# Kernel optimization log

Measured on AMD Instinct MI355X. Metric: run time of the kernel, lower is better.

## Reference

```python
import jax, jax.numpy as jnp
import numpy as np

EPS = 1e-5


def layer_norm(x, g, b):
    m = jnp.mean(x, axis=-1, keepdims=True)
    v = jnp.mean((x - m) ** 2, axis=-1, keepdims=True)
    return (x - m) / jnp.sqrt(v + EPS) * g + b


def rel_shift(x, klen):
    # x: [q, p, b, n] -> Transformer-XL relative shift -> [q, klen, b, n]
    q, p, b, n = x.shape
    x = jnp.reshape(x, (p, q, b, n))
    x = x[1:]
    x = jnp.reshape(x, (q, p - 1, b, n))
    return x[:, :klen]


def setup_inputs() -> dict:
    S, B, D, NH, DH, DF = 1024, 4, 1024, 16, 64, 4096
    key = jax.random.key(0)
    ks = jax.random.split(key, 16)
    w = 0.02  # scale random params for numerical sanity
    return {
        "src": jax.random.normal(ks[0], (S, B, D), jnp.float32),
        "pos_emb": jax.random.normal(ks[1], (S + 1, B, D), jnp.float32),
        "src_mask": jnp.zeros((S, S), dtype=bool),
        "qw": jax.random.normal(ks[2], (D, NH, DH), jnp.float32) * w,
        "kw": jax.random.normal(ks[3], (D, NH, DH), jnp.float32) * w,
        "vw": jax.random.normal(ks[4], (D, NH, DH), jnp.float32) * w,
        "rw": jax.random.normal(ks[5], (D, NH, DH), jnp.float32) * w,
        "ow": jax.random.normal(ks[6], (D, NH, DH), jnp.float32) * w,
        "r_w_bias": jax.random.normal(ks[7], (NH, DH), jnp.float32) * w,
        "r_r_bias": jax.random.normal(ks[8], (NH, DH), jnp.float32) * w,
        "w1": jax.random.normal(ks[9], (DF, D), jnp.float32) * w,
        "b1": jnp.zeros((DF,), jnp.float32),
        "w2": jax.random.normal(ks[10], (D, DF), jnp.float32) * w,
        "b2": jnp.zeros((D,), jnp.float32),
        "g1": jnp.ones((D,), jnp.float32),
        "beta1": jnp.zeros((D,), jnp.float32),
        "g2": jnp.ones((D,), jnp.float32),
        "beta2": jnp.zeros((D,), jnp.float32),
    }


def reference(src, pos_emb, src_mask, qw, kw, vw, rw, ow, r_w_bias, r_r_bias,
              w1, b1, w2, b2, g1, beta1, g2, beta2):
    S = src.shape[0]
    d_head = qw.shape[-1]
    scale = 1.0 / d_head ** 0.5

    # mem=None -> cat == src; dropout layers are identity (eval)
    q_head = jnp.einsum('ibh,hnd->ibnd', src, qw)
    k_head = jnp.einsum('ibh,hnd->ibnd', src, kw)
    v_head = jnp.einsum('ibh,hnd->ibnd', src, vw)
    k_pos = jnp.einsum('ibh,hnd->ibnd', pos_emb, rw)

    ac = jnp.einsum('ibnd,jbnd->ijbn', q_head + r_w_bias, k_head)       # [S,S,B,N]
    bd = jnp.einsum('ibnd,jbnd->ijbn', q_head + r_r_bias, k_pos)        # [S,S+1,B,N]
    bd = rel_shift(bd, klen=S)

    mask = src_mask.astype(ac.dtype)[:, :, None, None]
    attn_score = (ac + bd) * scale - 1e30 * mask
    attn_prob = jax.nn.softmax(attn_score, axis=1)

    attn_vec = jnp.einsum('ijbn,jbnd->ibnd', attn_prob, v_head)
    attn_out = jnp.einsum('ibnd,hnd->ibh', attn_vec, ow)

    x = layer_norm(src + attn_out, g1, beta1)
    ff = jax.nn.gelu(x @ w1.T + b1, approximate=False) @ w2.T + b2
    return layer_norm(x + ff, g2, beta2)
```

## Files before the change

### kernel.cpp

```cpp
#include <hip/hip_runtime.h>
#include <math.h>

typedef __bf16 bf16x8 __attribute__((ext_vector_type(8)));
typedef __bf16 bf16x4 __attribute__((ext_vector_type(4)));
typedef float f32x4 __attribute__((ext_vector_type(4)));

__device__ __forceinline__ void gload_lds16(const __bf16* g, __bf16* l) {
  __builtin_amdgcn_global_load_lds((const __attribute__((address_space(1))) void*)g,
                                   (__attribute__((address_space(3))) void*)l, 16, 0, 0);
}

__device__ __forceinline__ float gelu_exact(float v) {
  return 0.5f * v * (1.f + erff(v * 0.70710678118654752f));
}

__global__ __launch_bounds__(256) void prep_all(
    const float* __restrict__ src, __bf16* __restrict__ srcB2,
    const float* __restrict__ pos, __bf16* __restrict__ posB,
    const float* __restrict__ ow, __bf16* __restrict__ owB,
    const float* __restrict__ w1, __bf16* __restrict__ w1B,
    const float* __restrict__ w2, __bf16* __restrict__ w2B,
    const float* __restrict__ qw, const float* __restrict__ kw,
    const float* __restrict__ vw, const float* __restrict__ rw,
    __bf16* __restrict__ qkvT, __bf16* __restrict__ rwT) {
  __shared__ float t[32][33];
  int bid = blockIdx.x;
  const int tid = threadIdx.x;
  if (bid < 4096) {
    const int i = bid & 1023, b = bid >> 10;
    const float4 v = *(const float4*)(src + ((size_t)(i * 4 + b)) * 1024 + tid * 4);
    bf16x4 o = {(__bf16)v.x, (__bf16)v.y, (__bf16)v.z, (__bf16)v.w};
    *(bf16x4*)(srcB2 + (size_t)bid * 1024 + tid * 4) = o;
    return;
  }
  bid -= 4096;
  if (bid < 3329) {
    const float* in; __bf16* out;
    if (bid < 1025) { in = pos; out = posB; }
    else if (bid < 1281) { bid -= 1025; in = ow; out = owB; }
    else if (bid < 2305) { bid -= 1281; in = w1; out = w1B; }
    else { bid -= 2305; in = w2; out = w2B; }
    const int base = bid * 4096 + tid * 4;
#pragma unroll
    for (int k2 = 0; k2 < 4; ++k2) {
      const int off = base + k2 * 1024;
      float4 v = *(const float4*)(in + off);
      bf16x4 o = {(__bf16)v.x, (__bf16)v.y, (__bf16)v.z, (__bf16)v.w};
      *(bf16x4*)(out + off) = o;
    }
    return;
  }
  bid -= 3329;
  const int z = bid >> 10, rem = bid & 1023;
  const float* in; __bf16* out;
  switch (z) {
    case 0: in = qw; out = qkvT; break;
    case 1: in = kw; out = qkvT + 1024 * 1024; break;
    case 2: in = vw; out = qkvT + 2048 * 1024; break;
    default: in = rw; out = rwT; break;
  }
  const int c0 = (rem & 31) * 32, r0 = (rem >> 5) * 32;
  const int tx = tid & 31, ty = tid >> 5;
  for (int yy = ty; yy < 32; yy += 8)
    t[yy][tx] = in[(size_t)(r0 + yy) * 1024 + c0 + tx];
  __syncthreads();
  for (int yy = ty; yy < 32; yy += 8)
    out[(size_t)(c0 + yy) * 1024 + r0 + tx] = (__bf16)t[tx][yy];
}

template<int BM, int BN, int MODE>
__device__ __forceinline__ void gemm_body(
    const __bf16* __restrict__ A, const __bf16* __restrict__ BT,
    float* __restrict__ Cf, __bf16* __restrict__ Cb,
    const float* __restrict__ bias, int M, int N, int K,
    int kStart, int kChunk, int mBase, int nBase, char* smemRaw) {
  constexpr int BK = 32;
  constexpr int ALOAD = (BM * BK) / 2048;
  constexpr int BLOAD = (BN * BK) / 2048;
  __bf16* lA = (__bf16*)smemRaw;
  __bf16* lB = (__bf16*)(smemRaw + 4 * BM * BK);
  const int tid = threadIdx.x;
  const int w = tid >> 6, l = tid & 63;
  const int lr = l & 15, lk = l >> 4;
  const int srow = tid >> 2;
  const int scol = (tid & 3) * 8;
  const int wbase = w * 512;

  const __bf16* aSrc[ALOAD];
  const __bf16* bSrc[BLOAD];
#pragma unroll
  for (int i = 0; i < ALOAD; ++i) {
    int grow = mBase + srow + i * 64;
    grow = grow < M ? grow : M - 1;
    aSrc[i] = A + (size_t)grow * K + kStart + scol;
  }
#pragma unroll
  for (int i = 0; i < BLOAD; ++i) {
    const int grow = nBase + srow + i * 64;
    bSrc[i] = BT + (size_t)grow * K + kStart + scol;
  }
  auto stage = [&](int buf) {
#pragma unroll
    for (int i = 0; i < ALOAD; ++i) {
      gload_lds16(aSrc[i], &lA[buf * BM * BK + i * 2048 + wbase]);
      aSrc[i] += BK;
    }
#pragma unroll
    for (int i = 0; i < BLOAD; ++i) {
      gload_lds16(bSrc[i], &lB[buf * BN * BK + i * 2048 + wbase]);
      bSrc[i] += BK;
    }
  };

  constexpr int WM = BM / 2, WN = BN / 2;
  constexpr int MF = WM / 16, NF = WN / 16;
  const int wr = w >> 1, wc = w & 1;
  f32x4 acc[MF][NF] = {};

  const int nIter = kChunk / BK;
  stage(0);
  int cur = 0;
#pragma unroll 1
  for (int t = 0; t < nIter; ++t) {
    __syncthreads();
    if (t + 1 < nIter) stage(cur ^ 1);
    bf16x8 af[MF], bfr[NF];
#pragma unroll
    for (int mi = 0; mi < MF; ++mi)
      af[mi] = *(const bf16x8*)&lA[cur * BM * BK + (wr * WM + mi * 16 + lr) * BK + lk * 8];
#pragma unroll
    for (int nj = 0; nj < NF; ++nj)
      bfr[nj] = *(const bf16x8*)&lB[cur * BN * BK + (wc * WN + nj * 16 + lr) * BK + lk * 8];
#pragma unroll
    for (int mi = 0; mi < MF; ++mi)
#pragma unroll
      for (int nj = 0; nj < NF; ++nj)
        acc[mi][nj] = __builtin_amdgcn_mfma_f32_16x16x32_bf16(af[mi], bfr[nj], acc[mi][nj], 0, 0, 0);
    cur ^= 1;
  }
#pragma unroll
  for (int mi = 0; mi < MF; ++mi) {
#pragma unroll
    for (int nj = 0; nj < NF; ++nj) {
      const int col = nBase + wc * WN + nj * 16 + lr;
      const int row0 = mBase + wr * WM + mi * 16 + lk * 4;
#pragma unroll
      for (int j = 0; j < 4; ++j) {
        const int row = row0 + j;
        if (row < M) {
          float v = acc[mi][nj][j];
          if constexpr (MODE == 1) {
            v = gelu_exact(v + bias[col]);
            Cb[(size_t)row * N + col] = (__bf16)v;
          } else if constexpr (MODE == 2) {
            Cb[(size_t)row * N + col] = (__bf16)v;
          } else {
            Cf[(size_t)row * N + col] = v;
          }
        }
      }
    }
  }
}

template<int BM, int BN, int MODE>
__global__ __launch_bounds__(256)
void gemm_bt(const __bf16* __restrict__ A, const __bf16* __restrict__ BT,
             float* __restrict__ Cf, __bf16* __restrict__ Cb,
             __bf16* __restrict__ Cb2, const float* __restrict__ bias,
             int M, int N, int K, int kChunk) {
  __shared__ __align__(16) char smem[4 * (BM + BN) * 32];
  __bf16* cb = (blockIdx.z == 1) ? Cb2 : Cb;
  const int gx = gridDim.x;
  const int G = gx * gridDim.y;
  const int flat = blockIdx.y * gx + blockIdx.x;
  const int band = G >> 3;
  const int x8 = flat & 7, loc = flat >> 3;
  const int rpb = band / gx;
  const int ny = x8 * rpb + loc % rpb;
  const int nx = loc / rpb;
  gemm_body<BM, BN, MODE>(A, BT, Cf, cb, bias, M, N, K, blockIdx.z * kChunk,
                          kChunk, ny * BM, nx * BN, smem);
}

__global__ __launch_bounds__(256)
void proj3_kernel(const __bf16* __restrict__ srcB2, const __bf16* __restrict__ qkvT,
                  const __bf16* __restrict__ vwT, const __bf16* __restrict__ posB,
                  const __bf16* __restrict__ rwT, __bf16* __restrict__ qkB,
                  __bf16* __restrict__ vTB, __bf16* __restrict__ kposB) {
  __shared__ __align__(16) char smem[4 * (128 + 64) * 32];
  const int raw = blockIdx.x;
  int bid = (raw & 7) * 258 + (raw >> 3);
  if (bid < 1024) {
    gemm_body<128, 64, 2>(srcB2, qkvT, nullptr, qkB, nullptr, 4096, 2048, 1024,
                          0, 1024, (bid >> 5) * 128, (bid & 31) * 64, smem);
  } else if (bid < 1536) {
    const int t = bid - 1024;
    gemm_body<128, 64, 2>(vwT, srcB2, nullptr, vTB, nullptr, 1024, 4096, 1024,
                          0, 1024, (t >> 6) * 128, (t & 63) * 64, smem);
  } else {
    const int t = bid - 1536;
    gemm_body<128, 64, 2>(posB, rwT, nullptr, kposB, nullptr, 4100, 1024, 1024,
                          0, 1024, (t >> 4) * 128, (t & 15) * 64, smem);
  }
}

__global__ __launch_bounds__(256)
void attn8(const __bf16* __restrict__ qk, const __bf16* __restrict__ vT,
           const __bf16* __restrict__ kpos, const float* __restrict__ rwbias,
           const float* __restrict__ rrbias, __bf16* __restrict__ av) {
  constexpr float ALPHA = 0.125f * 1.44269504088896f;
  constexpr int PB = 132;
  __shared__ __align__(16) char smem[74240];
  __bf16* sP  = (__bf16*)(smem + 49152);
  __bf16* sbd = (__bf16*)(smem + 57344);

  const int flat = blockIdx.x;
  const int xcd = flat & 7, rr_ = flat >> 3;
  const int bn = xcd * 8 + (rr_ >> 4);
  const int it = rr_ & 15;
  const int b = bn >> 4, n = bn & 15;
  const int i0 = it * 64;
  const int tid = threadIdx.x;
  const int l = tid & 63;
  const int lcol = l & 15, lk = l >> 4;
  const int strip = (tid >> 6) * 16;
  const int wbase = tid & 192;
  const int nh64 = n * 64;
  const int q = strip + lcol;

  const int rB = tid >> 3;
  const int cs8 = ((tid & 7) ^ (rB & 7)) * 8;

  bf16x8 onesf;
#pragma unroll
  for (int u = 0; u < 8; ++u) onesf[u] = (__bf16)1.0f;

  bf16x8 qac[2], qlo[2], qhi[2];
  {
    const __bf16* qrow = qk + ((size_t)(b * 1024 + i0 + q)) * 2048 + nh64;
    int gH = i0 + q + 1; gH = gH < 1024 ? gH : 1023;
    const __bf16* qrowH = qk + ((size_t)(b * 1024 + gH)) * 2048 + nh64;
#pragma unroll
    for (int kk = 0; kk < 2; ++kk) {
      bf16x8 qv = *(const bf16x8*)(qrow + kk * 32 + lk * 8);
      bf16x8 qh = *(const bf16x8*)(qrowH + kk * 32 + lk * 8);
      const int dbase = nh64 + kk * 32 + lk * 8;
#pragma unroll
      for (int u = 0; u < 8; ++u) {
        const float rb = rrbias[dbase + u];
        qac[kk][u] = (__bf16)(((float)qv[u] + rwbias[dbase + u]) * ALPHA);
        qlo[kk][u] = (__bf16)(((float)qv[u] + rb) * ALPHA);
        qhi[kk][u] = (__bf16)(((float)qh[u] + rb) * ALPHA);
      }
    }
  }

#pragma unroll
  for (int kq = 0; kq < 2; ++kq) {
    const int r = kq * 32 + rB;
    const int dst = (kq * 256 + wbase) * 8;
    gload_lds16(kpos + ((size_t)((960 - i0 + r) * 4 + b)) * 1024 + nh64 + cs8,
                (__bf16*)(smem + 40960) + dst);
    gload_lds16(qk + ((size_t)(b * 1024 + r)) * 2048 + 1024 + nh64 + cs8,
                (__bf16*)(smem) + dst);
    const int rrel = r - i0;
    const int idx = (rrel <= 0) ? (1024 + rrel) : (rrel - 1);
    gload_lds16(kpos + ((size_t)(idx * 4 + b)) * 1024 + nh64 + cs8,
                (__bf16*)(smem + 16384) + dst);
    gload_lds16(vT + ((size_t)(nh64 + r)) * 4096 + b * 1024 + cs8,
                (__bf16*)(smem + 32768) + dst);
  }
  __syncthreads();
  {
    __bf16* kpl = (__bf16*)(smem + 40960);
    const int colb0 = (-i0 - 64) & 127;
#pragma unroll
    for (int fb = 0; fb < 4; ++fb) {
      const int row = fb * 16 + lcol;
      f32x4 g = {};
#pragma unroll
      for (int kk = 0; kk < 2; ++kk) {
        bf16x8 a = *(const bf16x8*)&kpl[row * 64 + (((kk * 4 + lk) ^ (lcol & 7)) * 8)];
        g = __builtin_amdgcn_mfma_f32_16x16x32_bf16(a, qlo[kk], g, 0, 0, 0);
      }
      bf16x4 gw = {(__bf16)g[0], (__bf16)g[1], (__bf16)g[2], (__bf16)g[3]};
      *(bf16x4*)&sbd[q * PB + ((colb0 + fb * 16 + lk * 4) & 127)] = gw;
    }
  }
  __syncthreads();

  f32x4 oacc[4] = {};
  f32x4 zq = {};
  size_t kS = (size_t)(b * 1024 + 64 + rB) * 2048 + 1024 + nh64 + cs8;
  size_t vS = (size_t)(nh64 + rB) * 4096 + b * 1024 + 64 + cs8;

#pragma unroll 1
  for (int jt = 0; jt < 16; ++jt) {
    const int cur = jt & 1, nxt = cur ^ 1;
    const int d0 = jt * 64 - i0;
    __bf16* sK   = (__bf16*)(smem + cur * 8192);
    __bf16* sKn  = (__bf16*)(smem + nxt * 8192);
    __bf16* sKP  = (__bf16*)(smem + 16384 + cur * 8192);
    __bf16* sKPn = (__bf16*)(smem + 16384 + nxt * 8192);
    __bf16* sVT  = (__bf16*)(smem + 32768 + cur * 8192);
    __bf16* sVTn = (__bf16*)(smem + 32768 + nxt * 8192);
#pragma unroll
    for (int kq = 0; kq < 2; ++kq) {
      const int dst = (kq * 256 + wbase) * 8;
      gload_lds16(qk + kS + kq * 65536, sKn + dst);
      gload_lds16(vT + vS + kq * 131072, sVTn + dst);
      const int rreln = d0 + 64 + kq * 32 + rB;
      const int idx = (rreln <= 0) ? (1024 + rreln) : (rreln - 1);
      gload_lds16(kpos + ((size_t)(idx * 4 + b)) * 1024 + nh64 + cs8, sKPn + dst);
    }
    kS += 131072; vS += 64;
    {
      const bf16x8 qg0 = (d0 >= 0) ? qhi[0] : qlo[0];
      const bf16x8 qg1 = (d0 >= 0) ? qhi[1] : qlo[1];
#pragma unroll
      for (int fb = 0; fb < 4; ++fb) {
        const int row = fb * 16 + lcol;
        f32x4 g = {};
        g = __builtin_amdgcn_mfma_f32_16x16x32_bf16(
            *(const bf16x8*)&sKP[row * 64 + ((lk ^ (lcol & 7)) * 8)], qg0, g, 0, 0, 0);
        g = __builtin_amdgcn_mfma_f32_16x16x32_bf16(
            *(const bf16x8*)&sKP[row * 64 + (((4 + lk) ^ (lcol & 7)) * 8)], qg1, g, 0, 0, 0);
        bf16x4 gw = {(__bf16)g[0], (__bf16)g[1], (__bf16)g[2], (__bf16)g[3]};
        *(bf16x4*)&sbd[q * PB + ((d0 + fb * 16 + lk * 4) & 127)] = gw;
      }
      if (d0 == 0) {
        const int cl = tid >> 2, part = tid & 3;
        const __bf16* qs = qk + ((size_t)(b * 1024 + i0 + cl)) * 2048 + nh64 + part * 16;
        bf16x8 a0 = *(const bf16x8*)qs;
        bf16x8 a1 = *(const bf16x8*)(qs + 8);
        bf16x8 k0 = *(const bf16x8*)&sKP[(2 * part) * 8];
        bf16x8 k1 = *(const bf16x8*)&sKP[(2 * part + 1) * 8];
        float s64 = 0.f;
#pragma unroll
        for (int u = 0; u < 8; ++u)
          s64 += ((float)a0[u] + rrbias[nh64 + part * 16 + u]) * (float)k0[u]
               + ((float)a1[u] + rrbias[nh64 + part * 16 + 8 + u]) * (float)k1[u];
        s64 += __shfl_xor(s64, 1, 64);
        s64 += __shfl_xor(s64, 2, 64);
        if (part == 0) sbd[cl * PB] = (__bf16)(s64 * ALPHA);
      }
    }
    f32x4 sc[4];
#pragma unroll
    for (int fk = 0; fk < 4; ++fk) {
      const int row = fk * 16 + lcol;
      f32x4 a = {};
#pragma unroll
      for (int kk = 0; kk < 2; ++kk) {
        bf16x8 kf = *(const bf16x8*)&sK[row * 64 + (((kk * 4 + lk) ^ (lcol & 7)) * 8)];
        a = __builtin_amdgcn_mfma_f32_16x16x32_bf16(kf, qac[kk], a, 0, 0, 0);
      }
      sc[fk] = a;
    }
    {
      const int rowb = q * PB;
      const int sb = d0 - q;
#pragma unroll
      for (int fk = 0; fk < 4; ++fk) {
        const int cb = sb + fk * 16 + lk * 4;
        float e0 = exp2f(sc[fk][0] + (float)sbd[rowb + ((cb) & 127)]);
        float e1 = exp2f(sc[fk][1] + (float)sbd[rowb + ((cb + 1) & 127)]);
        float e2 = exp2f(sc[fk][2] + (float)sbd[rowb + ((cb + 2) & 127)]);
        float e3 = exp2f(sc[fk][3] + (float)sbd[rowb + ((cb + 3) & 127)]);
        bf16x4 pw = {(__bf16)e0, (__bf16)e1, (__bf16)e2, (__bf16)e3};
        *(bf16x4*)&sP[q * 64 + (((fk * 2 + (lk >> 1)) ^ (q & 7)) * 8) + (lk & 1) * 4] = pw;
      }
    }
#pragma unroll
    for (int kk = 0; kk < 2; ++kk) {
      bf16x8 pa = *(const bf16x8*)&sP[q * 64 + (((kk * 4 + lk) ^ (q & 7)) * 8)];
      zq = __builtin_amdgcn_mfma_f32_16x16x32_bf16(pa, onesf, zq, 0, 0, 0);
#pragma unroll
      for (int fd = 0; fd < 4; ++fd) {
        const int vrow = fd * 16 + lcol;
        bf16x8 bv = *(const bf16x8*)&sVT[vrow * 64 + (((kk * 4 + lk) ^ (lcol & 7)) * 8)];
        oacc[fd] = __builtin_amdgcn_mfma_f32_16x16x32_bf16(pa, bv, oacc[fd], 0, 0, 0);
      }
    }
    __syncthreads();
  }
#pragma unroll
  for (int jj = 0; jj < 4; ++jj) {
    const float rz = 1.f / zq[jj];
    const int ig = i0 + strip + lk * 4 + jj;
    __bf16* dst = av + ((size_t)(ig * 4 + b)) * 1024 + nh64;
#pragma unroll
    for (int fd = 0; fd < 4; ++fd)
      dst[fd * 16 + lcol] = (__bf16)(oacc[fd][jj] * rz);
  }
}

__global__ __launch_bounds__(256)
void ln_fuse(const float* __restrict__ A, const __bf16* __restrict__ P0,
             const __bf16* __restrict__ P1, const float* __restrict__ cb,
             const float* __restrict__ g, const float* __restrict__ be,
             float* __restrict__ oF, __bf16* __restrict__ oB) {
  const int row = blockIdx.x, t = threadIdx.x;
  const size_t base = (size_t)row * 1024 + t * 4;
  const float4 a = *(const float4*)(A + base);
  const bf16x4 p0 = *(const bf16x4*)(P0 + base);
  const bf16x4 p1 = *(const bf16x4*)(P1 + base);
  float x0 = a.x + (float)p0[0] + (float)p1[0];
  float x1 = a.y + (float)p0[1] + (float)p1[1];
  float x2 = a.z + (float)p0[2] + (float)p1[2];
  float x3 = a.w + (float)p0[3] + (float)p1[3];
  if (cb) {
    const float4 c = *(const float4*)(cb + t * 4);
    x0 += c.x; x1 += c.y; x2 += c.z; x3 += c.w;
  }
  float s = x0 + x1 + x2 + x3;
  float qq = x0 * x0 + x1 * x1 + x2 * x2 + x3 * x3;
#pragma unroll
  for (int o = 1; o < 64; o <<= 1) { s += __shfl_xor(s, o, 64); qq += __shfl_xor(qq, o, 64); }
  __shared__ float ss[4], qs[4];
  if ((t & 63) == 0) { ss[t >> 6] = s; qs[t >> 6] = qq; }
  __syncthreads();
  s = ss[0] + ss[1] + ss[2] + ss[3];
  qq = qs[0] + qs[1] + qs[2] + qs[3];
  const float mean = s * (1.f / 1024.f);
  const float var = qq * (1.f / 1024.f) - mean * mean;
  const float rstd = rsqrtf(var + 1e-5f);
  const float4 gv = *(const float4*)(g + t * 4);
  const float4 bev = *(const float4*)(be + t * 4);
  const float y0 = (x0 - mean) * rstd * gv.x + bev.x;
  const float y1 = (x1 - mean) * rstd * gv.y + bev.y;
  const float y2 = (x2 - mean) * rstd * gv.z + bev.z;
  const float y3 = (x3 - mean) * rstd * gv.w + bev.w;
  if (oF) {
    float4 r = {y0, y1, y2, y3};
    *(float4*)(oF + base) = r;
  }
  if (oB) {
    bf16x4 o4 = {(__bf16)y0, (__bf16)y1, (__bf16)y2, (__bf16)y3};
    *(bf16x4*)(oB + base) = o4;
  }
}

extern "C" void kernel_launch(void* const* d_in, const int* in_sizes, int n_in,
                              void* d_out, int out_size, void* d_ws, size_t ws_size,
                              hipStream_t stream) {
  const float* src    = (const float*)d_in[0];
  const float* pos    = (const float*)d_in[1];
  const float* qw     = (const float*)d_in[3];
  const float* kw     = (const float*)d_in[4];
  const float* vw     = (const float*)d_in[5];
  const float* rw     = (const float*)d_in[6];
  const float* ow     = (const float*)d_in[7];
  const float* rwbias = (const float*)d_in[8];
  const float* rrbias = (const float*)d_in[9];
  const float* w1     = (const float*)d_in[10];
  const float* b1     = (const float*)d_in[11];
  const float* w2     = (const float*)d_in[12];
  const float* b2     = (const float*)d_in[13];
  const float* g1     = (const float*)d_in[14];
  const float* be1    = (const float*)d_in[15];
  const float* g2     = (const float*)d_in[16];
  const float* be2    = (const float*)d_in[17];
  float* out = (float*)d_out;

  char* p = (char*)d_ws;
  auto alloc = [&](size_t bytes) { char* r = p; p += (bytes + 255) & ~(size_t)255; return r; };
  __bf16* qkB   = (__bf16*)alloc(4096ull * 2048 * 2);
  __bf16* vTB   = (__bf16*)alloc(1024ull * 4096 * 2);
  __bf16* kposB = (__bf16*)alloc(4100ull * 1024 * 2);
  __bf16* avB   = (__bf16*)alloc(4096ull * 1024 * 2);
  __bf16* srcB2 = (__bf16*)alloc(4096ull * 1024 * 2);
  __bf16* posB  = (__bf16*)alloc(4100ull * 1024 * 2);
  float*  xF    = (float*)alloc(4096ull * 1024 * 4);
  __bf16* w2B   = (__bf16*)alloc(4096ull * 1024 * 2);
  __bf16* qkvT  = (__bf16*)alloc(3072ull * 1024 * 2);
  __bf16* rwT   = (__bf16*)alloc(1024ull * 1024 * 2);
  __bf16* owB   = (__bf16*)alloc(1024ull * 1024 * 2);
  __bf16* w1B   = (__bf16*)alloc(4096ull * 1024 * 2);
  __bf16* xB    = (__bf16*)alloc(4096ull * 1024 * 2);
  __bf16* gB   = qkB;
  __bf16* aoP0 = srcB2;
  __bf16* aoP1 = posB;
  __bf16* ffP0 = avB;
  __bf16* ffP1 = w1B;

  prep_all<<<11521, 256, 0, stream>>>(src, srcB2, pos, posB, ow, owB, w1, w1B,
                                      w2, w2B, qw, kw, vw, rw, qkvT, rwT);
  proj3_kernel<<<2064, 256, 0, stream>>>(srcB2, qkvT, qkvT + 2048 * 1024, posB,
                                         rwT, qkB, vTB, kposB);
  attn8<<<dim3(1024), 256, 0, stream>>>(qkB, vTB, kposB, rwbias, rrbias, avB);
  gemm_bt<128, 64, 2><<<dim3(16, 32, 2), 256, 0, stream>>>(avB, owB, nullptr, aoP0, aoP1, nullptr, 4096, 1024, 1024, 512);
  ln_fuse<<<4096, 256, 0, stream>>>(src, aoP0, aoP1, nullptr, g1, be1, xF, xB);
  gemm_bt<128, 64, 1><<<dim3(64, 32), 256, 0, stream>>>(xB, w1B, nullptr, gB, nullptr, b1, 4096, 4096, 1024, 1024);
  gemm_bt<128, 64, 2><<<dim3(16, 32, 2), 256, 0, stream>>>(gB, w2B, nullptr, ffP0, ffP1, nullptr, 4096, 1024, 4096, 2048);
  ln_fuse<<<4096, 256, 0, stream>>>(xF, ffP0, ffP1, b2, g2, be2, out, nullptr);
  (void)in_sizes; (void)n_in; (void)out_size; (void)ws_size;
}
```

Baseline: 318.2 us.

## Add 256x128 triple-buffered GEMM kernel for QK projection and FFN1

Adds a new 512-thread GEMM kernel with 256x128 output tiles, a three-stage LDS ring filled through global_load_lds, XOR-swizzled LDS layout, and interleaved prefetch issue. It is used for the fused Q/K projection and for the FFN up-projection with GELU. The V and positional projections move into a smaller separate kernel. Larger tiles raise operand reuse and cut global traffic, at the cost of fewer blocks (256 and 512), an extra kernel launch, and more register and LDS pressure.

```diff
diff --git a/kernel.cpp b/kernel.cpp
--- a/kernel.cpp
+++ b/kernel.cpp
@@ -184,25 +184,117 @@
 }
 
 __global__ __launch_bounds__(256)
-void proj3_kernel(const __bf16* __restrict__ srcB2, const __bf16* __restrict__ qkvT,
-                  const __bf16* __restrict__ vwT, const __bf16* __restrict__ posB,
-                  const __bf16* __restrict__ rwT, __bf16* __restrict__ qkB,
+void proj2_kernel(const __bf16* __restrict__ vwT, const __bf16* __restrict__ srcB2,
+                  const __bf16* __restrict__ posB, const __bf16* __restrict__ rwT,
                   __bf16* __restrict__ vTB, __bf16* __restrict__ kposB) {
   __shared__ __align__(16) char smem[4 * (128 + 64) * 32];
   const int raw = blockIdx.x;
-  int bid = (raw & 7) * 258 + (raw >> 3);
-  if (bid < 1024) {
-    gemm_body<128, 64, 2>(srcB2, qkvT, nullptr, qkB, nullptr, 4096, 2048, 1024,
-                          0, 1024, (bid >> 5) * 128, (bid & 31) * 64, smem);
-  } else if (bid < 1536) {
-    const int t = bid - 1024;
+  int bid = (raw & 7) * 130 + (raw >> 3);
+  if (bid < 512) {
     gemm_body<128, 64, 2>(vwT, srcB2, nullptr, vTB, nullptr, 1024, 4096, 1024,
-                          0, 1024, (t >> 6) * 128, (t & 63) * 64, smem);
+                          0, 1024, (bid >> 6) * 128, (bid & 63) * 64, smem);
   } else {
-    const int t = bid - 1536;
+    const int t = bid - 512;
     gemm_body<128, 64, 2>(posB, rwT, nullptr, kposB, nullptr, 4100, 1024, 1024,
                           0, 1024, (t >> 4) * 128, (t & 15) * 64, smem);
   }
+}
+
+template<int MODE>
+__global__ __launch_bounds__(512)
+void gemm256(const __bf16* __restrict__ A, const __bf16* __restrict__ BT,
+             __bf16* __restrict__ Cb, const float* __restrict__ bias,
+             int M, int N, int K) {
+  __shared__ __align__(16) __bf16 sm[3 * 24576];
+  const int tid = threadIdx.x;
+  const int wid = tid >> 6, l = tid & 63;
+  const int lcol = l & 15, lk = l >> 4;
+  const int wm = wid >> 1, wn = wid & 1;
+  const int gx = gridDim.x;
+  const int G = gx * gridDim.y;
+  const int flat = blockIdx.y * gx + blockIdx.x;
+  const int band = G >> 3;
+  const int x8 = flat & 7, loc = flat >> 3;
+  const int rpb = band / gx;
+  const int ny = x8 * rpb + loc % rpb;
+  const int nx = loc / rpb;
+  const int mBase = ny * 256, nBase = nx * 128;
+
+  int rowj[2], gslotj[2];
+#pragma unroll
+  for (int j = 0; j < 2; ++j) {
+    const int u = (wid * 2 + j) * 64 + l;
+    rowj[j] = u >> 3;
+    gslotj[j] = (u & 7) ^ (rowj[j] & 7);
+  }
+  auto issueHT = [&](int kt, int ht, int side) {
+    __bf16* base = sm + side * 24576 + (ht == 2 ? 16384 : ht * 8192);
+#pragma unroll
+    for (int j = 0; j < 2; ++j) {
+      const __bf16* src = (ht < 2)
+        ? A + (size_t)(mBase + ht * 128 + rowj[j]) * K + kt * 64 + gslotj[j] * 8
+        : BT + (size_t)(nBase + rowj[j]) * K + kt * 64 + gslotj[j] * 8;
+      gload_lds16(src, base + (wid * 2 + j) * 512);
+    }
+  };
+
+  const int nkt = K >> 6;
+  issueHT(0, 0, 0); issueHT(0, 1, 0); issueHT(0, 2, 0);
+  issueHT(1, 0, 1); issueHT(1, 1, 1); issueHT(1, 2, 1);
+
+  f32x4 acc[4][4] = {};
+#pragma unroll 1
+  for (int j = 0; j < nkt; ++j) {
+    asm volatile("s_waitcnt vmcnt(6)" ::: "memory");
+    __builtin_amdgcn_s_barrier();
+    __builtin_amdgcn_sched_barrier(0);
+    const int side = j % 3;
+    const int sn = (j + 2) % 3;
+    const int ktn = (j + 2 < nkt) ? j + 2 : nkt - 1;
+    const __bf16* Ab = sm + side * 24576;
+    const __bf16* Bb = Ab + 16384;
+    issueHT(ktn, 0, sn);
+    bf16x8 af[4][2];
+#pragma unroll
+    for (int mi = 0; mi < 4; ++mi)
+#pragma unroll
+      for (int kk = 0; kk < 2; ++kk) {
+        const int row = wm * 64 + mi * 16 + lcol;
+        af[mi][kk] = *(const bf16x8*)&Ab[row * 64 + (((kk * 4 + lk) ^ (row & 7)) * 8)];
+      }
+    issueHT(ktn, 1, sn);
+    bf16x8 bfv[4][2];
+#pragma unroll
+    for (int nj = 0; nj < 4; ++nj)
+#pragma unroll
+      for (int kk = 0; kk < 2; ++kk) {
+        const int row = wn * 64 + nj * 16 + lcol;
+        bfv[nj][kk] = *(const bf16x8*)&Bb[row * 64 + (((kk * 4 + lk) ^ (row & 7)) * 8)];
+      }
+    issueHT(ktn, 2, sn);
+    __builtin_amdgcn_s_setprio(1);
+#pragma unroll
+    for (int mi = 0; mi < 4; ++mi)
+#pragma unroll
+      for (int nj = 0; nj < 4; ++nj) {
+        acc[mi][nj] = __builtin_amdgcn_mfma_f32_16x16x32_bf16(af[mi][0], bfv[nj][0], acc[mi][nj], 0, 0, 0);
+        acc[mi][nj] = __builtin_amdgcn_mfma_f32_16x16x32_bf16(af[mi][1], bfv[nj][1], acc[mi][nj], 0, 0, 0);
+      }
+    __builtin_amdgcn_s_setprio(0);
+  }
+#pragma unroll
+  for (int mi = 0; mi < 4; ++mi)
+#pragma unroll
+    for (int nj = 0; nj < 4; ++nj) {
+      const int col = nBase + wn * 64 + nj * 16 + lcol;
+      const int row0 = mBase + wm * 64 + mi * 16 + lk * 4;
+#pragma unroll
+      for (int jj = 0; jj < 4; ++jj) {
+        float v = acc[mi][nj][jj];
+        if constexpr (MODE == 1) v = gelu_exact(v + bias[col]);
+        Cb[(size_t)(row0 + jj) * N + col] = (__bf16)v;
+      }
+    }
 }
 
 __global__ __launch_bounds__(256)
@@ -487,12 +579,12 @@
 
   prep_all<<<11521, 256, 0, stream>>>(src, srcB2, pos, posB, ow, owB, w1, w1B,
                                       w2, w2B, qw, kw, vw, rw, qkvT, rwT);
-  proj3_kernel<<<2064, 256, 0, stream>>>(srcB2, qkvT, qkvT + 2048 * 1024, posB,
-                                         rwT, qkB, vTB, kposB);
+  gemm256<2><<<dim3(16, 16), 512, 0, stream>>>(srcB2, qkvT, qkB, nullptr, 4096, 2048, 1024);
+  proj2_kernel<<<1040, 256, 0, stream>>>(qkvT + 2048 * 1024, srcB2, posB, rwT, vTB, kposB);
   attn8<<<dim3(1024), 256, 0, stream>>>(qkB, vTB, kposB, rwbias, rrbias, avB);
   gemm_bt<128, 64, 2><<<dim3(16, 32, 2), 256, 0, stream>>>(avB, owB, nullptr, aoP0, aoP1, nullptr, 4096, 1024, 1024, 512);
   ln_fuse<<<4096, 256, 0, stream>>>(src, aoP0, aoP1, nullptr, g1, be1, xF, xB);
-  gemm_bt<128, 64, 1><<<dim3(64, 32), 256, 0, stream>>>(xB, w1B, nullptr, gB, nullptr, b1, 4096, 4096, 1024, 1024);
+  gemm256<1><<<dim3(32, 16), 512, 0, stream>>>(xB, w1B, gB, b1, 4096, 4096, 1024);
   gemm_bt<128, 64, 2><<<dim3(16, 32, 2), 256, 0, stream>>>(gB, w2B, nullptr, ffP0, ffP1, nullptr, 4096, 1024, 4096, 2048);
   ln_fuse<<<4096, 256, 0, stream>>>(xF, ffP0, ffP1, b2, g2, be2, out, nullptr);
   (void)in_sizes; (void)n_in; (void)out_size; (void)ws_size;
```

Measured after the change: 317.9 us. Within noise of the previous version (-0.1%).
